# Optimization experiments

Hardware: AMD Instinct MI355X
Metric: run time of the kernel (lower is better)

## Reference

```python
import jax, jax.numpy as jnp
import numpy as np

B, CIN, H, W = 16, 256, 56, 56
D, HEADS, KS, PAD, STRIDE, M = 256, 8, 3, 1, 1, 4
K = KS * KS
N = D // HEADS
# relative_indices: sum of window coords, flattened row-major, values in [0, 2*KS-2]
REL = (np.arange(KS)[:, None] + np.arange(KS)[None, :]).reshape(-1)


def setup_inputs() -> dict:
    key = jax.random.key(0)
    ks = jax.random.split(key, 7)
    return {
        "x": jax.random.normal(ks[0], (B, CIN, H, W), jnp.float32),
        "q": jax.random.normal(ks[1], (B, D, 1), jnp.float32),
        "Wk": jax.random.normal(ks[2], (D, CIN), jnp.float32) * 0.05,
        "Wv": jax.random.normal(ks[3], (D, CIN), jnp.float32) * 0.05,
        "pos_emb": jax.random.normal(ks[4], (1, 2 * KS - 1), jnp.float32),
        "Wlin": jax.random.normal(ks[5], (1, M), jnp.float32),
        "Wproj": jax.random.normal(ks[6], (D, D), jnp.float32) * 0.05,
    }


def _unfold(t):
    # torch nn.Unfold: (B,C,H,W) -> (B, C*K, L); patches feature dim ordered (C, kh, kw)
    p = jax.lax.conv_general_dilated_patches(
        t, (KS, KS), (STRIDE, STRIDE), [(PAD, PAD), (PAD, PAD)])
    b, _, ho, wo = p.shape
    return p.reshape(b, -1, ho * wo), ho, wo


def reference(x, q, Wk, Wv, pos_emb, Wlin, Wproj):
    b = x.shape[0]
    k = jnp.einsum('oc,bchw->bohw', Wk, x)  # 1x1 conv, no bias
    v = jnp.einsum('oc,bchw->bohw', Wv, x)
    ku, ho, wo = _unfold(k)
    vu, _, _ = _unfold(v)
    L = ho * wo
    ku = ku.reshape(b, HEADS, N, K, L)  # (b, h, n, k, l)
    vu = vu.reshape(b, HEADS, N, K, L)
    qh = q.reshape(b, HEADS, N)  # learned per-batch query, d=1 squeezed
    attn = jnp.einsum('bhn,bhnkl->bhlk', qh, ku)  # (b,h,l,K)
    attn = attn + pos_emb[0, REL]  # relative position bias, shape (K,)
    attn = jax.nn.softmax(attn, axis=-1)
    # repeat d(=1) -> m identical rows then Linear(m,1,no bias): equals scale by sum(Wlin)
    attn = attn * jnp.sum(Wlin)
    out = jnp.einsum('bhlk,bhnkl->bhnl', attn, vu)  # (b,h,n,l)
    out = out.reshape(b, D, ho, wo)  # fold with kernel 1 == reshape
    return jnp.einsum('oc,bchw->bohw', Wproj, out)  # 1x1 proj conv
```

## Files before the change

### kernel.cpp

```cpp
#include <hip/hip_runtime.h>

#define B_     16
#define D_     256
#define HEADS_ 8
#define N_     32
#define H_     56
#define W_     56
#define L_     3136
#define LDA    40

typedef short short8 __attribute__((ext_vector_type(8)));
typedef float f32x4  __attribute__((ext_vector_type(4)));

__device__ __forceinline__ unsigned short f2bf(float f) {
    union { float f; unsigned u; } c; c.f = f;
    unsigned u = c.u;
    u += 0x7fffu + ((u >> 16) & 1u);
    return (unsigned short)(u >> 16);
}

__global__ __launch_bounds__(256) void transpose_x_kernel(
    const float* __restrict__ x, unsigned short* __restrict__ Xt)
{
    __shared__ float tile[64][65];
    const int bb = blockIdx.z;
    const int c0 = blockIdx.y * 64;
    const int l0 = blockIdx.x * 64;
    const int t  = threadIdx.x;
    const int g4 = (t & 15) * 4;
    const int rr = t >> 4;

    const float* xb = x + ((size_t)bb * D_ + c0) * L_ + l0;
#pragma unroll
    for (int i = 0; i < 4; ++i) {
        const int c = rr + i * 16;
        float4 v = *(const float4*)(xb + (size_t)c * L_ + g4);
        *(float4*)&tile[c][g4] = v;
    }
    __syncthreads();
    unsigned short* Xb = Xt + ((size_t)bb * L_ + l0) * D_ + c0;
#pragma unroll
    for (int i = 0; i < 4; ++i) {
        const int l = rr + i * 16;
        uint2 o;
        o.x = (unsigned)f2bf(tile[g4 + 0][l]) | ((unsigned)f2bf(tile[g4 + 1][l]) << 16);
        o.y = (unsigned)f2bf(tile[g4 + 2][l]) | ((unsigned)f2bf(tile[g4 + 3][l]) << 16);
        *(uint2*)(Xb + (size_t)l * D_ + g4) = o;
    }
}

__global__ __launch_bounds__(256) void convert_w_kernel(
    const float* __restrict__ w0, const float* __restrict__ w1,
    const float* __restrict__ w2, unsigned short* __restrict__ o0,
    unsigned short* __restrict__ o1, unsigned short* __restrict__ o2)
{
    const float* src; unsigned short* dst;
    if (blockIdx.y == 0)      { src = w0; dst = o0; }
    else if (blockIdx.y == 1) { src = w1; dst = o1; }
    else                      { src = w2; dst = o2; }
    const int i = (blockIdx.x * 256 + threadIdx.x) * 4;
    float4 v = *(const float4*)(src + i);
    uint2 o;
    o.x = (unsigned)f2bf(v.x) | ((unsigned)f2bf(v.y) << 16);
    o.y = (unsigned)f2bf(v.z) | ((unsigned)f2bf(v.w) << 16);
    *(uint2*)(dst + i) = o;
}

__global__ __launch_bounds__(256) void gemm_kv_mfma(
    const unsigned short* __restrict__ Xt, const unsigned short* __restrict__ Wkb,
    const unsigned short* __restrict__ Wvb, const float* __restrict__ q,
    unsigned short* __restrict__ Vo, float* __restrict__ S)
{
    __shared__ unsigned short Aks[128][LDA];
    __shared__ unsigned short Avs[128][LDA];
    __shared__ unsigned short Bs[64][LDA];

    const int bb = blockIdx.z;
    const int d0 = blockIdx.y * 128;
    const int l0 = blockIdx.x * 64;
    const int t  = threadIdx.x;
    const int w    = t >> 6;
    const int lane = t & 63;
    const int col  = lane & 15;
    const int quad = lane >> 4;

    f32x4 accK[2][4], accV[2][4];
#pragma unroll
    for (int mi = 0; mi < 2; ++mi)
#pragma unroll
        for (int ni = 0; ni < 4; ++ni) {
            accK[mi][ni] = (f32x4){0.f, 0.f, 0.f, 0.f};
            accV[mi][ni] = (f32x4){0.f, 0.f, 0.f, 0.f};
        }

    const int srow = t >> 2;
    const int skc  = (t & 3) * 8;
    const unsigned short* Xrow = Xt + ((size_t)bb * L_ + l0 + srow) * D_ + skc;
    const unsigned short* Wk0  = Wkb + (size_t)(d0 + srow) * D_ + skc;
    const unsigned short* Wk1  = Wkb + (size_t)(d0 + 64 + srow) * D_ + skc;
    const unsigned short* Wv0  = Wvb + (size_t)(d0 + srow) * D_ + skc;
    const unsigned short* Wv1  = Wvb + (size_t)(d0 + 64 + srow) * D_ + skc;

    for (int kt = 0; kt < 8; ++kt) {
        const int c0 = kt * 32;
        uint4 xg  = *(const uint4*)(Xrow + c0);
        uint4 kg0 = *(const uint4*)(Wk0 + c0);
        uint4 kg1 = *(const uint4*)(Wk1 + c0);
        uint4 vg0 = *(const uint4*)(Wv0 + c0);
        uint4 vg1 = *(const uint4*)(Wv1 + c0);

        __syncthreads();
        *(uint4*)&Bs[srow][skc]        = xg;
        *(uint4*)&Aks[srow][skc]       = kg0;
        *(uint4*)&Aks[srow + 64][skc]  = kg1;
        *(uint4*)&Avs[srow][skc]       = vg0;
        *(uint4*)&Avs[srow + 64][skc]  = vg1;
        __syncthreads();

        short8 ak0 = *(const short8*)&Aks[w * 32 + col][quad * 8];
        short8 ak1 = *(const short8*)&Aks[w * 32 + 16 + col][quad * 8];
        short8 av0 = *(const short8*)&Avs[w * 32 + col][quad * 8];
        short8 av1 = *(const short8*)&Avs[w * 32 + 16 + col][quad * 8];
        short8 bfr[4];
#pragma unroll
        for (int ni = 0; ni < 4; ++ni)
            bfr[ni] = *(const short8*)&Bs[ni * 16 + col][quad * 8];

#pragma unroll
        for (int ni = 0; ni < 4; ++ni) {
            accK[0][ni] = __builtin_amdgcn_mfma_f32_16x16x32_bf16(ak0, bfr[ni], accK[0][ni], 0, 0, 0);
            accK[1][ni] = __builtin_amdgcn_mfma_f32_16x16x32_bf16(ak1, bfr[ni], accK[1][ni], 0, 0, 0);
            accV[0][ni] = __builtin_amdgcn_mfma_f32_16x16x32_bf16(av0, bfr[ni], accV[0][ni], 0, 0, 0);
            accV[1][ni] = __builtin_amdgcn_mfma_f32_16x16x32_bf16(av1, bfr[ni], accV[1][ni], 0, 0, 0);
        }
    }

#pragma unroll
    for (int mi = 0; mi < 2; ++mi)
#pragma unroll
        for (int ni = 0; ni < 4; ++ni)
#pragma unroll
            for (int r = 0; r < 4; ++r) {
                const int d = d0 + w * 32 + mi * 16 + quad * 4 + r;
                const int l = l0 + ni * 16 + col;
                Vo[((size_t)bb * D_ + d) * L_ + l] = f2bf(accV[mi][ni][r]);
            }

    const int hh = blockIdx.y * 4 + w;
    float qv[2][4];
#pragma unroll
    for (int mi = 0; mi < 2; ++mi)
#pragma unroll
        for (int r = 0; r < 4; ++r)
            qv[mi][r] = q[bb * D_ + hh * N_ + mi * 16 + quad * 4 + r];

#pragma unroll
    for (int ni = 0; ni < 4; ++ni) {
        float s = 0.f;
#pragma unroll
        for (int mi = 0; mi < 2; ++mi)
#pragma unroll
            for (int r = 0; r < 4; ++r)
                s = fmaf(qv[mi][r], accK[mi][ni][r], s);
        s += __shfl_xor(s, 16, 64);
        s += __shfl_xor(s, 32, 64);
        if (lane < 16)
            S[((size_t)bb * HEADS_ + hh) * L_ + l0 + ni * 16 + col] = s;
    }
}

__global__ __launch_bounds__(256) void attend_kernel(
    const float* __restrict__ S, const unsigned short* __restrict__ Vo,
    const float* __restrict__ pos_emb, const float* __restrict__ Wlin,
    unsigned short* __restrict__ Om)
{
    __shared__ unsigned short Vs[10][60][8];
    __shared__ float Ss[10][58];

    const int band = blockIdx.x;
    const int half = blockIdx.y;
    const int bh   = blockIdx.z;
    const int y0   = band * 8;
    const int t    = threadIdx.x;

    const float* Sb = S + (size_t)bh * L_;
    for (int wi = t; wi < 580; wi += 256) {
        const int row = wi / 58, c = wi - row * 58;
        const int gr = y0 - 1 + row, gc = c - 1;
        float v = 0.f;
        if (gr >= 0 && gr < H_ && gc >= 0 && gc < W_)
            v = Sb[gr * W_ + gc];
        Ss[row][c] = v;
    }

    const unsigned short* Vbase = Vo + ((size_t)bh * N_ + half * 8) * L_;
    for (int j = t; j < 560; j += 256) {
        const int ch = j & 7;
        const int rr = j >> 3;
        const int row = rr / 7, cg = rr - row * 7;
        const int gr = y0 - 1 + row;
        uint4 v = make_uint4(0u, 0u, 0u, 0u);
        if (gr >= 0 && gr < H_)
            v = *(const uint4*)(Vbase + (size_t)ch * L_ + gr * W_ + cg * 8);
        const unsigned short* hw = (const unsigned short*)&v;
        const int colb = cg * 8 + 1;
#pragma unroll
        for (int i = 0; i < 8; ++i)
            Vs[row][colb + i][ch] = hw[i];
    }
    if (t < 160) {
        const int row = t >> 4, side = (t >> 3) & 1, ch = t & 7;
        Vs[row][side ? 57 : 0][ch] = 0;
    }
    __syncthreads();

    const float scale = Wlin[0] + Wlin[1] + Wlin[2] + Wlin[3];
    const float pe0 = pos_emb[0], pe1 = pos_emb[1], pe2 = pos_emb[2];
    const float pe3 = pos_emb[3], pe4 = pos_emb[4];
    const float bias[9] = {pe0, pe1, pe2, pe1, pe2, pe3, pe2, pe3, pe4};

    for (int p = t; p < 448; p += 256) {
        const int yl = p / 56, xx = p - yl * 56;
        const int lr = yl + 1, lc = xx + 1;

        float lg[9], m = -1e30f;
#pragma unroll
        for (int dy = 0; dy < 3; ++dy)
#pragma unroll
            for (int dx = 0; dx < 3; ++dx) {
                const int k = dy * 3 + dx;
                lg[k] = Ss[lr - 1 + dy][lc - 1 + dx] + bias[k];
                m = fmaxf(m, lg[k]);
            }
        float ssum = 0.f;
#pragma unroll
        for (int k = 0; k < 9; ++k) { lg[k] = __expf(lg[k] - m); ssum += lg[k]; }
        const float inv = scale / ssum;

        float om[8] = {0.f, 0.f, 0.f, 0.f, 0.f, 0.f, 0.f, 0.f};
#pragma unroll
        for (int dy = 0; dy < 3; ++dy)
#pragma unroll
            for (int dx = 0; dx < 3; ++dx) {
                const float wk = lg[dy * 3 + dx] * inv;
                const uint4 v = *(const uint4*)&Vs[lr - 1 + dy][lc - 1 + dx][0];
                const unsigned* u = (const unsigned*)&v;
#pragma unroll
                for (int i = 0; i < 4; ++i) {
                    union { unsigned uu; float f; } lo, hi;
                    lo.uu = u[i] << 16;
                    hi.uu = u[i] & 0xffff0000u;
                    om[2 * i]     = fmaf(wk, lo.f, om[2 * i]);
                    om[2 * i + 1] = fmaf(wk, hi.f, om[2 * i + 1]);
                }
            }

        unsigned short ob[8];
#pragma unroll
        for (int i = 0; i < 8; ++i) ob[i] = f2bf(om[i]);
        const int l = (y0 + yl) * W_ + xx;
        *(uint4*)(Om + ((size_t)bh * L_ + l) * N_ + half * 8) = *(const uint4*)ob;
    }
}

__global__ __launch_bounds__(256) void gemm_proj_mfma(
    const unsigned short* __restrict__ Om, const unsigned short* __restrict__ Wpb,
    float* __restrict__ Out)
{
    __shared__ unsigned short As[128][LDA];
    __shared__ unsigned short Bs[64][LDA];

    const int bb = blockIdx.z;
    const int d0 = blockIdx.y * 128;
    const int l0 = blockIdx.x * 64;
    const int t  = threadIdx.x;
    const int w    = t >> 6;
    const int lane = t & 63;
    const int col  = lane & 15;
    const int quad = lane >> 4;

    f32x4 acc[2][4];
#pragma unroll
    for (int mi = 0; mi < 2; ++mi)
#pragma unroll
        for (int ni = 0; ni < 4; ++ni) acc[mi][ni] = (f32x4){0.f, 0.f, 0.f, 0.f};

    const int srow = t >> 2;
    const int skc  = (t & 3) * 8;
    const unsigned short* Wp0 = Wpb + (size_t)(d0 + srow) * D_ + skc;
    const unsigned short* Wp1 = Wpb + (size_t)(d0 + 64 + srow) * D_ + skc;
    const unsigned short* Orow = Om + ((size_t)bb * HEADS_ * L_ + l0 + srow) * N_ + skc;

    for (int kt = 0; kt < 8; ++kt) {
        const int c0 = kt * 32;
        uint4 bg  = *(const uint4*)(Orow + (size_t)kt * L_ * N_);
        uint4 ag0 = *(const uint4*)(Wp0 + c0);
        uint4 ag1 = *(const uint4*)(Wp1 + c0);

        __syncthreads();
        *(uint4*)&Bs[srow][skc]       = bg;
        *(uint4*)&As[srow][skc]       = ag0;
        *(uint4*)&As[srow + 64][skc]  = ag1;
        __syncthreads();

        short8 a0 = *(const short8*)&As[w * 32 + col][quad * 8];
        short8 a1 = *(const short8*)&As[w * 32 + 16 + col][quad * 8];
        short8 bfr[4];
#pragma unroll
        for (int ni = 0; ni < 4; ++ni)
            bfr[ni] = *(const short8*)&Bs[ni * 16 + col][quad * 8];

#pragma unroll
        for (int ni = 0; ni < 4; ++ni) {
            acc[0][ni] = __builtin_amdgcn_mfma_f32_16x16x32_bf16(a0, bfr[ni], acc[0][ni], 0, 0, 0);
            acc[1][ni] = __builtin_amdgcn_mfma_f32_16x16x32_bf16(a1, bfr[ni], acc[1][ni], 0, 0, 0);
        }
    }

#pragma unroll
    for (int mi = 0; mi < 2; ++mi)
#pragma unroll
        for (int ni = 0; ni < 4; ++ni)
#pragma unroll
            for (int r = 0; r < 4; ++r) {
                const int d = d0 + w * 32 + mi * 16 + quad * 4 + r;
                const int l = l0 + ni * 16 + col;
                Out[((size_t)bb * D_ + d) * L_ + l] = acc[mi][ni][r];
            }
}

extern "C" void kernel_launch(void* const* d_in, const int* in_sizes, int n_in,
                              void* d_out, int out_size, void* d_ws, size_t ws_size,
                              hipStream_t stream)
{
    const float* x       = (const float*)d_in[0];
    const float* q       = (const float*)d_in[1];
    const float* Wk      = (const float*)d_in[2];
    const float* Wv      = (const float*)d_in[3];
    const float* pos_emb = (const float*)d_in[4];
    const float* Wlin    = (const float*)d_in[5];
    const float* Wproj   = (const float*)d_in[6];
    float* out = (float*)d_out;

    const size_t planeE = (size_t)B_ * D_ * L_;
    unsigned short* Xt  = (unsigned short*)d_ws;
    unsigned short* Vo  = Xt + planeE;
    unsigned short* Om  = Vo + planeE;
    unsigned short* Wkb = Om + planeE;
    unsigned short* Wvb = Wkb + D_ * D_;
    unsigned short* Wpb = Wvb + D_ * D_;
    float*          S   = (float*)(Wpb + D_ * D_);

    transpose_x_kernel<<<dim3(L_ / 64, D_ / 64, B_), 256, 0, stream>>>(x, Xt);
    convert_w_kernel<<<dim3(64, 3), 256, 0, stream>>>(Wk, Wv, Wproj, Wkb, Wvb, Wpb);
    gemm_kv_mfma<<<dim3(L_ / 64, 2, B_), 256, 0, stream>>>(Xt, Wkb, Wvb, q, Vo, S);
    attend_kernel<<<dim3(7, 4, B_ * HEADS_), 256, 0, stream>>>(
        S, Vo, pos_emb, Wlin, Om);
    gemm_proj_mfma<<<dim3(L_ / 64, 2, B_), 256, 0, stream>>>(Om, Wpb, out);
}
```

Measured before the change: 181.1 us.

## Fuse x transpose into KV GEMM, widen tiles to full D, relayout V as channel-last

Removes the separate transpose/convert kernel for x: the KV GEMM now loads fp32 x directly, stages it in shared memory and converts it to bf16 while building the B fragments. Each block now covers all 256 output channels (grid y dimension drops from 2 to 1), and weight fragments are read straight from global memory into registers instead of going through shared memory. V is written in a per-head channel-last layout so the attend kernel can load it with one vector load per pixel, which simplifies its halo handling. The projection GEMM gets the same full-D tiling. This cuts one full read and write of a bf16 copy of x and one kernel launch, at the cost of more registers (4x4 accumulators for both K and V), strided scalar shared-memory reads during the conversion, and fewer blocks in the grid.

```diff
diff --git a/kernel.cpp b/kernel.cpp
--- a/kernel.cpp
+++ b/kernel.cpp
@@ -7,7 +7,8 @@
 #define H_     56
 #define W_     56
 #define L_     3136
-#define LDA    40
+#define LDB    40
+#define LDX    66
 
 typedef short short8 __attribute__((ext_vector_type(8)));
 typedef float f32x4  __attribute__((ext_vector_type(4)));
@@ -17,36 +18,6 @@
     unsigned u = c.u;
     u += 0x7fffu + ((u >> 16) & 1u);
     return (unsigned short)(u >> 16);
-}
-
-__global__ __launch_bounds__(256) void transpose_x_kernel(
-    const float* __restrict__ x, unsigned short* __restrict__ Xt)
-{
-    __shared__ float tile[64][65];
-    const int bb = blockIdx.z;
-    const int c0 = blockIdx.y * 64;
-    const int l0 = blockIdx.x * 64;
-    const int t  = threadIdx.x;
-    const int g4 = (t & 15) * 4;
-    const int rr = t >> 4;
-
-    const float* xb = x + ((size_t)bb * D_ + c0) * L_ + l0;
-#pragma unroll
-    for (int i = 0; i < 4; ++i) {
-        const int c = rr + i * 16;
-        float4 v = *(const float4*)(xb + (size_t)c * L_ + g4);
-        *(float4*)&tile[c][g4] = v;
-    }
-    __syncthreads();
-    unsigned short* Xb = Xt + ((size_t)bb * L_ + l0) * D_ + c0;
-#pragma unroll
-    for (int i = 0; i < 4; ++i) {
-        const int l = rr + i * 16;
-        uint2 o;
-        o.x = (unsigned)f2bf(tile[g4 + 0][l]) | ((unsigned)f2bf(tile[g4 + 1][l]) << 16);
-        o.y = (unsigned)f2bf(tile[g4 + 2][l]) | ((unsigned)f2bf(tile[g4 + 3][l]) << 16);
-        *(uint2*)(Xb + (size_t)l * D_ + g4) = o;
-    }
 }
 
 __global__ __launch_bounds__(256) void convert_w_kernel(
@@ -66,17 +37,14 @@
     *(uint2*)(dst + i) = o;
 }
 
-__global__ __launch_bounds__(256) void gemm_kv_mfma(
-    const unsigned short* __restrict__ Xt, const unsigned short* __restrict__ Wkb,
+__global__ __launch_bounds__(256, 2) void gemm_kv_mfma(
+    const float* __restrict__ x, const unsigned short* __restrict__ Wkb,
     const unsigned short* __restrict__ Wvb, const float* __restrict__ q,
     unsigned short* __restrict__ Vo, float* __restrict__ S)
 {
-    __shared__ unsigned short Aks[128][LDA];
-    __shared__ unsigned short Avs[128][LDA];
-    __shared__ unsigned short Bs[64][LDA];
+    __shared__ float Xs[32][LDX];
 
     const int bb = blockIdx.z;
-    const int d0 = blockIdx.y * 128;
     const int l0 = blockIdx.x * 64;
     const int t  = threadIdx.x;
     const int w    = t >> 6;
@@ -84,88 +52,98 @@
     const int col  = lane & 15;
     const int quad = lane >> 4;
 
-    f32x4 accK[2][4], accV[2][4];
-#pragma unroll
-    for (int mi = 0; mi < 2; ++mi)
+    f32x4 accK[4][4], accV[4][4];
+#pragma unroll
+    for (int mi = 0; mi < 4; ++mi)
 #pragma unroll
         for (int ni = 0; ni < 4; ++ni) {
             accK[mi][ni] = (f32x4){0.f, 0.f, 0.f, 0.f};
             accV[mi][ni] = (f32x4){0.f, 0.f, 0.f, 0.f};
         }
 
-    const int srow = t >> 2;
-    const int skc  = (t & 3) * 8;
-    const unsigned short* Xrow = Xt + ((size_t)bb * L_ + l0 + srow) * D_ + skc;
-    const unsigned short* Wk0  = Wkb + (size_t)(d0 + srow) * D_ + skc;
-    const unsigned short* Wk1  = Wkb + (size_t)(d0 + 64 + srow) * D_ + skc;
-    const unsigned short* Wv0  = Wvb + (size_t)(d0 + srow) * D_ + skc;
-    const unsigned short* Wv1  = Wvb + (size_t)(d0 + 64 + srow) * D_ + skc;
+    const int xc = t >> 3;
+    const int xl = (t & 7) * 8;
+    const float* xrow = x + ((size_t)bb * D_ + xc) * L_ + l0 + xl;
+
+    const unsigned short* wk0 = Wkb + (size_t)(w * 64 + col) * D_ + quad * 8;
+    const unsigned short* wv0 = Wvb + (size_t)(w * 64 + col) * D_ + quad * 8;
 
     for (int kt = 0; kt < 8; ++kt) {
         const int c0 = kt * 32;
-        uint4 xg  = *(const uint4*)(Xrow + c0);
-        uint4 kg0 = *(const uint4*)(Wk0 + c0);
-        uint4 kg1 = *(const uint4*)(Wk1 + c0);
-        uint4 vg0 = *(const uint4*)(Wv0 + c0);
-        uint4 vg1 = *(const uint4*)(Wv1 + c0);
+        const float* xp = xrow + (size_t)c0 * L_;
+        float4 x0 = *(const float4*)xp;
+        float4 x1 = *(const float4*)(xp + 4);
+        short8 ak[4], av[4];
+#pragma unroll
+        for (int mi = 0; mi < 4; ++mi) {
+            ak[mi] = *(const short8*)(wk0 + (size_t)mi * 16 * D_ + c0);
+            av[mi] = *(const short8*)(wv0 + (size_t)mi * 16 * D_ + c0);
+        }
 
         __syncthreads();
-        *(uint4*)&Bs[srow][skc]        = xg;
-        *(uint4*)&Aks[srow][skc]       = kg0;
-        *(uint4*)&Aks[srow + 64][skc]  = kg1;
-        *(uint4*)&Avs[srow][skc]       = vg0;
-        *(uint4*)&Avs[srow + 64][skc]  = vg1;
+        *(float2*)&Xs[xc][xl + 0] = make_float2(x0.x, x0.y);
+        *(float2*)&Xs[xc][xl + 2] = make_float2(x0.z, x0.w);
+        *(float2*)&Xs[xc][xl + 4] = make_float2(x1.x, x1.y);
+        *(float2*)&Xs[xc][xl + 6] = make_float2(x1.z, x1.w);
         __syncthreads();
 
-        short8 ak0 = *(const short8*)&Aks[w * 32 + col][quad * 8];
-        short8 ak1 = *(const short8*)&Aks[w * 32 + 16 + col][quad * 8];
-        short8 av0 = *(const short8*)&Avs[w * 32 + col][quad * 8];
-        short8 av1 = *(const short8*)&Avs[w * 32 + 16 + col][quad * 8];
         short8 bfr[4];
 #pragma unroll
         for (int ni = 0; ni < 4; ++ni)
-            bfr[ni] = *(const short8*)&Bs[ni * 16 + col][quad * 8];
-
+#pragma unroll
+            for (int j = 0; j < 8; ++j)
+                bfr[ni][j] = (short)f2bf(Xs[quad * 8 + j][ni * 16 + col]);
+
+#pragma unroll
+        for (int mi = 0; mi < 4; ++mi)
+#pragma unroll
+            for (int ni = 0; ni < 4; ++ni) {
+                accK[mi][ni] = __builtin_amdgcn_mfma_f32_16x16x32_bf16(ak[mi], bfr[ni], accK[mi][ni], 0, 0, 0);
+                accV[mi][ni] = __builtin_amdgcn_mfma_f32_16x16x32_bf16(av[mi], bfr[ni], accV[mi][ni], 0, 0, 0);
+            }
+    }
+
+#pragma unroll
+    for (int mi = 0; mi < 4; ++mi) {
+        const int hh = w * 2 + (mi >> 1);
+        const int dn = (mi & 1) * 16 + quad * 4;
 #pragma unroll
         for (int ni = 0; ni < 4; ++ni) {
-            accK[0][ni] = __builtin_amdgcn_mfma_f32_16x16x32_bf16(ak0, bfr[ni], accK[0][ni], 0, 0, 0);
-            accK[1][ni] = __builtin_amdgcn_mfma_f32_16x16x32_bf16(ak1, bfr[ni], accK[1][ni], 0, 0, 0);
-            accV[0][ni] = __builtin_amdgcn_mfma_f32_16x16x32_bf16(av0, bfr[ni], accV[0][ni], 0, 0, 0);
-            accV[1][ni] = __builtin_amdgcn_mfma_f32_16x16x32_bf16(av1, bfr[ni], accV[1][ni], 0, 0, 0);
-        }
-    }
-
-#pragma unroll
-    for (int mi = 0; mi < 2; ++mi)
-#pragma unroll
-        for (int ni = 0; ni < 4; ++ni)
-#pragma unroll
-            for (int r = 0; r < 4; ++r) {
-                const int d = d0 + w * 32 + mi * 16 + quad * 4 + r;
-                const int l = l0 + ni * 16 + col;
-                Vo[((size_t)bb * D_ + d) * L_ + l] = f2bf(accV[mi][ni][r]);
-            }
-
-    const int hh = blockIdx.y * 4 + w;
-    float qv[2][4];
-#pragma unroll
-    for (int mi = 0; mi < 2; ++mi)
+            unsigned short pk[4];
+#pragma unroll
+            for (int r = 0; r < 4; ++r) pk[r] = f2bf(accV[mi][ni][r]);
+            const int l = l0 + ni * 16 + col;
+            *(uint2*)(Vo + ((((size_t)(bb * HEADS_ + hh)) * L_ + l) << 5) + dn) =
+                *(const uint2*)pk;
+        }
+    }
+
+    float qv[4][4];
+#pragma unroll
+    for (int mi = 0; mi < 4; ++mi)
 #pragma unroll
         for (int r = 0; r < 4; ++r)
-            qv[mi][r] = q[bb * D_ + hh * N_ + mi * 16 + quad * 4 + r];
+            qv[mi][r] = q[bb * D_ + w * 64 + mi * 16 + quad * 4 + r];
 
 #pragma unroll
     for (int ni = 0; ni < 4; ++ni) {
-        float s = 0.f;
-#pragma unroll
-        for (int mi = 0; mi < 2; ++mi)
-#pragma unroll
-            for (int r = 0; r < 4; ++r)
-                s = fmaf(qv[mi][r], accK[mi][ni][r], s);
-        s += __shfl_xor(s, 16, 64);
-        s += __shfl_xor(s, 32, 64);
-        if (lane < 16)
-            S[((size_t)bb * HEADS_ + hh) * L_ + l0 + ni * 16 + col] = s;
+        float s0 = 0.f, s1 = 0.f;
+#pragma unroll
+        for (int r = 0; r < 4; ++r) {
+            s0 = fmaf(qv[0][r], accK[0][ni][r], s0);
+            s0 = fmaf(qv[1][r], accK[1][ni][r], s0);
+            s1 = fmaf(qv[2][r], accK[2][ni][r], s1);
+            s1 = fmaf(qv[3][r], accK[3][ni][r], s1);
+        }
+        s0 += __shfl_xor(s0, 16, 64);
+        s0 += __shfl_xor(s0, 32, 64);
+        s1 += __shfl_xor(s1, 16, 64);
+        s1 += __shfl_xor(s1, 32, 64);
+        if (lane < 16) {
+            const int l = l0 + ni * 16 + col;
+            S[(size_t)(bb * HEADS_ + w * 2) * L_ + l]     = s0;
+            S[(size_t)(bb * HEADS_ + w * 2 + 1) * L_ + l] = s1;
+        }
     }
 }
 
@@ -174,7 +152,7 @@
     const float* __restrict__ pos_emb, const float* __restrict__ Wlin,
     unsigned short* __restrict__ Om)
 {
-    __shared__ unsigned short Vs[10][60][8];
+    __shared__ unsigned short Vs[10][58][8];
     __shared__ float Ss[10][58];
 
     const int band = blockIdx.x;
@@ -184,33 +162,15 @@
     const int t    = threadIdx.x;
 
     const float* Sb = S + (size_t)bh * L_;
-    for (int wi = t; wi < 580; wi += 256) {
-        const int row = wi / 58, c = wi - row * 58;
+    for (int j = t; j < 580; j += 256) {
+        const int row = j / 58, c = j - row * 58;
         const int gr = y0 - 1 + row, gc = c - 1;
-        float v = 0.f;
-        if (gr >= 0 && gr < H_ && gc >= 0 && gc < W_)
-            v = Sb[gr * W_ + gc];
-        Ss[row][c] = v;
-    }
-
-    const unsigned short* Vbase = Vo + ((size_t)bh * N_ + half * 8) * L_;
-    for (int j = t; j < 560; j += 256) {
-        const int ch = j & 7;
-        const int rr = j >> 3;
-        const int row = rr / 7, cg = rr - row * 7;
-        const int gr = y0 - 1 + row;
-        uint4 v = make_uint4(0u, 0u, 0u, 0u);
-        if (gr >= 0 && gr < H_)
-            v = *(const uint4*)(Vbase + (size_t)ch * L_ + gr * W_ + cg * 8);
-        const unsigned short* hw = (const unsigned short*)&v;
-        const int colb = cg * 8 + 1;
-#pragma unroll
-        for (int i = 0; i < 8; ++i)
-            Vs[row][colb + i][ch] = hw[i];
-    }
-    if (t < 160) {
-        const int row = t >> 4, side = (t >> 3) & 1, ch = t & 7;
-        Vs[row][side ? 57 : 0][ch] = 0;
+        const bool in = (gr >= 0 && gr < H_ && gc >= 0 && gc < W_);
+        Ss[row][c] = in ? Sb[gr * W_ + gc] : 0.f;
+        uint4 vv = make_uint4(0u, 0u, 0u, 0u);
+        if (in)
+            vv = *(const uint4*)(Vo + (((size_t)bh * L_ + gr * W_ + gc) << 5) + half * 8);
+        *(uint4*)&Vs[row][c][0] = vv;
     }
     __syncthreads();
 
@@ -259,19 +219,17 @@
 #pragma unroll
         for (int i = 0; i < 8; ++i) ob[i] = f2bf(om[i]);
         const int l = (y0 + yl) * W_ + xx;
-        *(uint4*)(Om + ((size_t)bh * L_ + l) * N_ + half * 8) = *(const uint4*)ob;
-    }
-}
-
-__global__ __launch_bounds__(256) void gemm_proj_mfma(
+        *(uint4*)(Om + (((size_t)bh * L_ + l) << 5) + half * 8) = *(const uint4*)ob;
+    }
+}
+
+__global__ __launch_bounds__(256, 2) void gemm_proj_mfma(
     const unsigned short* __restrict__ Om, const unsigned short* __restrict__ Wpb,
     float* __restrict__ Out)
 {
-    __shared__ unsigned short As[128][LDA];
-    __shared__ unsigned short Bs[64][LDA];
+    __shared__ unsigned short Bs[64][LDB];
 
     const int bb = blockIdx.z;
-    const int d0 = blockIdx.y * 128;
     const int l0 = blockIdx.x * 64;
     const int t  = threadIdx.x;
     const int w    = t >> 6;
@@ -279,51 +237,48 @@
     const int col  = lane & 15;
     const int quad = lane >> 4;
 
-    f32x4 acc[2][4];
-#pragma unroll
-    for (int mi = 0; mi < 2; ++mi)
+    f32x4 acc[4][4];
+#pragma unroll
+    for (int mi = 0; mi < 4; ++mi)
 #pragma unroll
         for (int ni = 0; ni < 4; ++ni) acc[mi][ni] = (f32x4){0.f, 0.f, 0.f, 0.f};
 
     const int srow = t >> 2;
     const int skc  = (t & 3) * 8;
-    const unsigned short* Wp0 = Wpb + (size_t)(d0 + srow) * D_ + skc;
-    const unsigned short* Wp1 = Wpb + (size_t)(d0 + 64 + srow) * D_ + skc;
-    const unsigned short* Orow = Om + ((size_t)bb * HEADS_ * L_ + l0 + srow) * N_ + skc;
+    const unsigned short* wp0 = Wpb + (size_t)(w * 64 + col) * D_ + quad * 8;
 
     for (int kt = 0; kt < 8; ++kt) {
         const int c0 = kt * 32;
-        uint4 bg  = *(const uint4*)(Orow + (size_t)kt * L_ * N_);
-        uint4 ag0 = *(const uint4*)(Wp0 + c0);
-        uint4 ag1 = *(const uint4*)(Wp1 + c0);
+        uint4 bg = *(const uint4*)(Om +
+            ((((size_t)(bb * HEADS_ + kt)) * L_ + l0 + srow) << 5) + skc);
+        short8 a[4];
+#pragma unroll
+        for (int mi = 0; mi < 4; ++mi)
+            a[mi] = *(const short8*)(wp0 + (size_t)mi * 16 * D_ + c0);
 
         __syncthreads();
-        *(uint4*)&Bs[srow][skc]       = bg;
-        *(uint4*)&As[srow][skc]       = ag0;
-        *(uint4*)&As[srow + 64][skc]  = ag1;
+        *(uint4*)&Bs[srow][skc] = bg;
         __syncthreads();
 
-        short8 a0 = *(const short8*)&As[w * 32 + col][quad * 8];
-        short8 a1 = *(const short8*)&As[w * 32 + 16 + col][quad * 8];
         short8 bfr[4];
 #pragma unroll
         for (int ni = 0; ni < 4; ++ni)
             bfr[ni] = *(const short8*)&Bs[ni * 16 + col][quad * 8];
 
 #pragma unroll
-        for (int ni = 0; ni < 4; ++ni) {
-            acc[0][ni] = __builtin_amdgcn_mfma_f32_16x16x32_bf16(a0, bfr[ni], acc[0][ni], 0, 0, 0);
-            acc[1][ni] = __builtin_amdgcn_mfma_f32_16x16x32_bf16(a1, bfr[ni], acc[1][ni], 0, 0, 0);
-        }
-    }
-
-#pragma unroll
-    for (int mi = 0; mi < 2; ++mi)
+        for (int mi = 0; mi < 4; ++mi)
+#pragma unroll
+            for (int ni = 0; ni < 4; ++ni)
+                acc[mi][ni] = __builtin_amdgcn_mfma_f32_16x16x32_bf16(a[mi], bfr[ni], acc[mi][ni], 0, 0, 0);
+    }
+
+#pragma unroll
+    for (int mi = 0; mi < 4; ++mi)
 #pragma unroll
         for (int ni = 0; ni < 4; ++ni)
 #pragma unroll
             for (int r = 0; r < 4; ++r) {
-                const int d = d0 + w * 32 + mi * 16 + quad * 4 + r;
+                const int d = w * 64 + mi * 16 + quad * 4 + r;
                 const int l = l0 + ni * 16 + col;
                 Out[((size_t)bb * D_ + d) * L_ + l] = acc[mi][ni][r];
             }
@@ -343,18 +298,16 @@
     float* out = (float*)d_out;
 
     const size_t planeE = (size_t)B_ * D_ * L_;
-    unsigned short* Xt  = (unsigned short*)d_ws;
-    unsigned short* Vo  = Xt + planeE;
+    unsigned short* Vo  = (unsigned short*)d_ws;
     unsigned short* Om  = Vo + planeE;
     unsigned short* Wkb = Om + planeE;
     unsigned short* Wvb = Wkb + D_ * D_;
     unsigned short* Wpb = Wvb + D_ * D_;
     float*          S   = (float*)(Wpb + D_ * D_);
 
-    transpose_x_kernel<<<dim3(L_ / 64, D_ / 64, B_), 256, 0, stream>>>(x, Xt);
     convert_w_kernel<<<dim3(64, 3), 256, 0, stream>>>(Wk, Wv, Wproj, Wkb, Wvb, Wpb);
-    gemm_kv_mfma<<<dim3(L_ / 64, 2, B_), 256, 0, stream>>>(Xt, Wkb, Wvb, q, Vo, S);
+    gemm_kv_mfma<<<dim3(L_ / 64, 1, B_), 256, 0, stream>>>(x, Wkb, Wvb, q, Vo, S);
     attend_kernel<<<dim3(7, 4, B_ * HEADS_), 256, 0, stream>>>(
         S, Vo, pos_emb, Wlin, Om);
-    gemm_proj_mfma<<<dim3(L_ / 64, 2, B_), 256, 0, stream>>>(Om, Wpb, out);
-}
+    gemm_proj_mfma<<<dim3(L_ / 64, 1, B_), 256, 0, stream>>>(Om, Wpb, out);
+}
```

Measured after the change: 195.7 us. 1.08x slower.
